# Kernel optimization log

Measured on AMD Instinct MI355X. Metric: run time of the kernel, lower is better.

The kernel has to match this reference:

```python
import jax, jax.numpy as jnp
import numpy as np

B, Q, A, D = 32, 48, 48, 300   # batch, question len, answer len, word embed dim
C, K = 512, 5                  # conv out channels, kernel height
H, P, NCLS = 512, 512, 2       # hidden_size, projection_size, n_classes
EPS_COS = 1e-6
EPS_BN = 1e-5


def _simple_cnn(x, conv_w, conv_b, fc_w, fc_b):
    # x: (N, L, D) -> Conv2d(1->C, kernel=(K, D), padding=(K-1, 0)) -> relu -> maxpool over length -> fc
    y = jax.lax.conv_general_dilated(
        x[:, None, :, :], conv_w, window_strides=(1, 1),
        padding=((K - 1, K - 1), (0, 0)),
        dimension_numbers=('NCHW', 'OIHW', 'NCHW'))  # (N, C, L+K-1, 1)
    y = jax.nn.relu(y + conv_b[None, :, None, None])[..., 0]  # (N, C, L')
    y = jnp.max(y, axis=2)                                    # (N, C)  max_pool1d over full length
    return y @ fc_w.T + fc_b                                  # (N, H)


def setup_inputs() -> dict:
    key = jax.random.key(0)
    ks = jax.random.split(key, 12)
    s = lambda n: 1.0 / np.sqrt(n)
    return {
        'a_features': jax.random.normal(ks[0], (B, Q, D), jnp.float32),
        'b_features': jax.random.normal(ks[1], (B, A, D), jnp.float32),
        'sm_conv_w': jax.random.normal(ks[2], (C, 1, K, D), jnp.float32) * s(K * D),
        'sm_conv_b': jnp.zeros((C,), jnp.float32),
        'sm_fc_w': jax.random.normal(ks[3], (H, C), jnp.float32) * s(C),
        'sm_fc_b': jnp.zeros((H,), jnp.float32),
        'ctx_conv_w': jax.random.normal(ks[4], (C, 1, K, D), jnp.float32) * s(K * D),
        'ctx_conv_b': jnp.zeros((C,), jnp.float32),
        'ctx_fc_w': jax.random.normal(ks[5], (H, C), jnp.float32) * s(C),
        'ctx_fc_b': jnp.zeros((H,), jnp.float32),
        'proj_w': jax.random.normal(ks[6], (P, 3 * H), jnp.float32) * s(3 * H),
        'proj_b': jnp.zeros((P,), jnp.float32),
        'bn_gamma': jnp.ones((P,), jnp.float32),
        'bn_beta': jnp.zeros((P,), jnp.float32),
        'out_w': jax.random.normal(ks[7], (NCLS, P), jnp.float32) * s(P),
        'out_b': jnp.zeros((NCLS,), jnp.float32),
    }


def reference(a_features, b_features, sm_conv_w, sm_conv_b, sm_fc_w, sm_fc_b,
              ctx_conv_w, ctx_conv_b, ctx_fc_w, ctx_fc_b,
              proj_w, proj_b, bn_gamma, bn_beta, out_w, out_b):
    q, a = a_features, b_features
    a_cnn = _simple_cnn(q, sm_conv_w, sm_conv_b, sm_fc_w, sm_fc_b)  # (B, H)
    b_cnn = _simple_cnn(a, sm_conv_w, sm_conv_b, sm_fc_w, sm_fc_b)  # (B, H)

    # attn_context_ave: cosine sim between every (question pos, answer pos) pair
    qn = jnp.linalg.norm(q, axis=-1)                # (B, Q)
    an = jnp.linalg.norm(a, axis=-1)                # (B, A)
    dots = jnp.einsum('bqd,bad->bqa', q, a)
    cos = dots / jnp.maximum(qn[:, :, None] * an[:, None, :], EPS_COS)  # (B, Q, A)
    attn_answer = (a[:, None, :, :] * cos[..., None]).reshape(B * Q, A, D)
    feat = _simple_cnn(attn_answer, ctx_conv_w, ctx_conv_b, ctx_fc_w, ctx_fc_b)
    attn_feat = jnp.mean(feat.reshape(B, Q, H), axis=1)  # sum/Q == mean, (B, H)

    comb = jnp.concatenate([a_cnn, b_cnn, attn_feat], axis=1)  # (B, 3H)
    comb = comb @ proj_w.T + proj_b                            # (B, P)
    # BatchNorm1d in training mode (batch statistics, biased variance)
    mu = jnp.mean(comb, axis=0)
    var = jnp.mean((comb - mu) ** 2, axis=0)
    comb = (comb - mu) / jnp.sqrt(var + EPS_BN) * bn_gamma + bn_beta
    logits = jnp.tanh(comb) @ out_w.T + out_b                  # (B, NCLS)
    return logits
```

## Files before the change

kernel.cpp:

```cpp
#include <hip/hip_runtime.h>
#include <math.h>
#include <stdint.h>

namespace {
constexpr int B = 32, Q = 48, A = 48, D = 300;
constexpr int C = 512, K = 5, H = 512, P = 512, NCLS = 2;
constexpr int CK = C * K;
constexpr int M = B * Q;
constexpr int KP = 320;
constexpr float EPS_COS = 1e-6f, EPS_BN = 1e-5f;
constexpr int NPAN = 96 + 96 + 160 + 160;
constexpr int NCOS = M / 4;
constexpr int NTP  = 768 + 512;
constexpr int NJ = 8;
constexpr int PSZ = 40 * 16 * 8;
}
using short8 = __attribute__((ext_vector_type(8))) short;
using f32x4  = __attribute__((ext_vector_type(4))) float;

__device__ inline short f2bf(float v) {
  uint32_t u = __builtin_bit_cast(uint32_t, v);
  return (short)((u + 0x7fffu + ((u >> 16) & 1u)) >> 16);
}

__global__ void prep_k(const float* __restrict__ q, const float* __restrict__ a,
                       const float* __restrict__ smw, const float* __restrict__ ctxw,
                       const float* __restrict__ projw, const float* __restrict__ smfcw,
                       const float* __restrict__ ctxfcw,
                       short* __restrict__ qb, short* __restrict__ ab,
                       short* __restrict__ smb, short* __restrict__ ctxb,
                       float* __restrict__ projT, float* __restrict__ smfcwT,
                       float* __restrict__ ctxfcwT, float* __restrict__ cosm) {
  __shared__ float sa[16 * 300];
  __shared__ float4 qrow4[300];
  __shared__ float tile[32][33];
  const int vb = blockIdx.x, tid = threadIdx.x;
  if (vb < NPAN) {
    const float* src; short* dst; int pl;
    if (vb < 96)       { src = q;    dst = qb;   pl = vb; }
    else if (vb < 192) { src = a;    dst = ab;   pl = vb - 96; }
    else if (vb < 352) { src = smw;  dst = smb;  pl = vb - 192; }
    else               { src = ctxw; dst = ctxb; pl = vb - 352; }
    const int row0 = pl * 16;
    for (int i = tid; i < 1200; i += 256) {
      const int r = i / 75, c4 = i - r * 75;
      const float4 v = *(const float4*)&src[(size_t)(row0 + r) * D + c4 * 4];
      *(float4*)&sa[r * 300 + c4 * 4] = v;
    }
    __syncthreads();
    for (int it = tid; it < 640; it += 256) {
      const int k8 = it >> 4, r = it & 15;
      short tmp[8];
#pragma unroll
      for (int e = 0; e < 8; ++e) {
        const int k = k8 * 8 + e;
        tmp[e] = (k < D) ? f2bf(sa[r * 300 + k]) : (short)0;
      }
      *(int4*)&dst[(size_t)pl * PSZ + (size_t)k8 * 128 + r * 8] = *(const int4*)tmp;
    }
  } else if (vb < NPAN + NCOS) {
    const int b5 = vb - NPAN;
    const int qq = b5 * 4;
    const int b = qq / Q;
    const float4* qp4 = (const float4*)(q + (size_t)qq * D);
    for (int i = tid; i < 300; i += 256) qrow4[i] = qp4[i];
    __syncthreads();
    const int sub = tid >> 6, lane = tid & 63;
    float qsq = 0.f;
    for (int i = lane; i < 75; i += 64) {
      float4 v = qrow4[sub * 75 + i];
      qsq += v.x * v.x + v.y * v.y + v.z * v.z + v.w * v.w;
    }
#pragma unroll
    for (int off2 = 32; off2; off2 >>= 1) qsq += __shfl_xor(qsq, off2);
    const float qn = sqrtf(qsq);
    if (lane < A) {
      const float4* ap4 = (const float4*)(a + ((size_t)b * A + lane) * D);
      float dot = 0.f, asq = 0.f;
      for (int i = 0; i < 75; ++i) {
        float4 av = ap4[i], qv = qrow4[sub * 75 + i];
        dot += qv.x * av.x + qv.y * av.y + qv.z * av.z + qv.w * av.w;
        asq += av.x * av.x + av.y * av.y + av.z * av.z + av.w * av.w;
      }
      cosm[(size_t)(qq + sub) * A + lane] = dot / fmaxf(qn * sqrtf(asq), EPS_COS);
    }
  } else {
    const int vb2 = vb - NPAN - NCOS;
    const int tx = tid & 31, ty = tid >> 5;
    if (vb2 < 768) {
      const int j0 = (vb2 % 48) * 32, p0 = (vb2 / 48) * 32;
      for (int i = ty; i < 32; i += 8)
        tile[i][tx] = projw[(size_t)(p0 + i) * (3 * H) + j0 + tx];
      __syncthreads();
      for (int i = ty; i < 32; i += 8)
        projT[(size_t)(j0 + i) * P + p0 + tx] = tile[tx][i];
    } else {
      const int b3 = vb2 - 768;
      const bool isC = b3 >= 256;
      const int b4 = isC ? b3 - 256 : b3;
      const float* W = isC ? ctxfcw : smfcw;
      float* WT = isC ? ctxfcwT : smfcwT;
      const int c0 = (b4 % 16) * 32, h0 = (b4 / 16) * 32;
      for (int i = ty; i < 32; i += 8)
        tile[i][tx] = W[(size_t)(h0 + i) * C + c0 + tx];
      __syncthreads();
      for (int i = ty; i < 32; i += 8)
        WT[(size_t)(c0 + i) * H + h0 + tx] = tile[tx][i];
    }
  }
}

__global__ void __launch_bounds__(256)
fused_k(const short* __restrict__ qb, const short* __restrict__ ab,
        const short* __restrict__ smb, const short* __restrict__ ctxb,
        const float* __restrict__ cosm, const float* __restrict__ smbias,
        const float* __restrict__ ctxbias,
        float* __restrict__ pooled, float* __restrict__ pbar) {
  __shared__ __align__(16) char Lraw[80000];
  const int vb = blockIdx.x, tid = threadIdx.x;

  float (*Sl)[56][81] = (float (*)[56][81])Lraw;
  short (*coslb)[56]  = (short (*)[56])(Lraw + 72576);
  float* redf         = (float*)(Lraw + 77952);
  const bool isCtx = vb < 256;
  const int lane = tid & 63, wv = tid >> 6;
  const int r16 = lane & 15, kq = lane >> 4;
  const int v2 = isCtx ? vb : vb - 256;
  const int nb = v2 >> 3, cgi = v2 & 7;

  const short* Xp = isCtx ? ab : ((nb < B) ? qb : ab);
  const int xp0 = (isCtx ? nb : ((nb < B) ? nb : nb - B)) * 3;
  const short* Wp = isCtx ? ctxb : smb;
  const int wp0 = cgi * 20 + wv * 5;
  const short* Xw = Xp + (size_t)xp0 * PSZ + kq * 128 + r16 * 8;
  const short* Ww = Wp + (size_t)wp0 * PSZ + kq * 128 + r16 * 8;

  for (int i = lane; i < 640; i += 64) {
    const int rr = i / 80, cc2 = i % 80;
    Sl[wv][rr < 4 ? rr : rr + 48][cc2] = 0.f;
  }
  if (isCtx) {
    for (int i = tid; i < 48 * 56; i += 256) {
      const int qi = i / 56, p4 = i % 56;
      const float cv = (p4 >= 4 && p4 < 52)
                     ? cosm[((size_t)nb * Q + qi) * A + p4 - 4] : 0.f;
      coslb[qi][p4] = f2bf(cv);
    }
  }

  f32x4 acc[3][5];
#pragma unroll
  for (int mi = 0; mi < 3; ++mi)
#pragma unroll
    for (int ni = 0; ni < 5; ++ni) acc[mi][ni] = f32x4{0.f, 0.f, 0.f, 0.f};

  int4 cA0[3], cB0[5], cA1[3], cB1[5], cA2[3], cB2[5];
  auto issue = [&](int ks, int4* pA, int4* pB) {
#pragma unroll
    for (int i = 0; i < 3; ++i) pA[i] = *(const int4*)(Xw + (size_t)i * PSZ + ks * 512);
#pragma unroll
    for (int i = 0; i < 5; ++i) pB[i] = *(const int4*)(Ww + (size_t)i * PSZ + ks * 512);
  };
  auto domfma = [&](const int4* pA, const int4* pB) {
#pragma unroll
    for (int mi = 0; mi < 3; ++mi)
#pragma unroll
      for (int ni = 0; ni < 5; ++ni)
        acc[mi][ni] = __builtin_amdgcn_mfma_f32_16x16x32_bf16(
            __builtin_bit_cast(short8, pA[mi]),
            __builtin_bit_cast(short8, pB[ni]), acc[mi][ni], 0, 0, 0);
  };

  issue(0, cA0, cB0);
  issue(1, cA1, cB1);
  issue(2, cA2, cB2);
  domfma(cA0, cB0); issue(3, cA0, cB0);
  domfma(cA1, cB1); issue(4, cA1, cB1);
  domfma(cA2, cB2); issue(5, cA2, cB2);
  domfma(cA0, cB0); issue(6, cA0, cB0);
  domfma(cA1, cB1); issue(7, cA1, cB1);
  domfma(cA2, cB2); issue(8, cA2, cB2);
  domfma(cA0, cB0); issue(9, cA0, cB0);
  domfma(cA1, cB1);
  domfma(cA2, cB2);
  domfma(cA0, cB0);

#pragma unroll
  for (int mi = 0; mi < 3; ++mi)
#pragma unroll
    for (int ni = 0; ni < 5; ++ni)
#pragma unroll
      for (int r = 0; r < 4; ++r)
        Sl[wv][mi * 16 + kq * 4 + r + 4][ni * 16 + r16] = acc[mi][ni][r];
  __syncthreads();

  if (!isCtx) {
    const int ch = tid & 63, part = tid >> 6;
    const int w2 = ch >> 4, cl = (ch & 15) * 5;
    float best = -1e30f;
#pragma unroll
    for (int j = 0; j < 13; ++j) {
      const int l = part * 13 + j;
      const float z = Sl[w2][l + 0][cl + 0] + Sl[w2][l + 1][cl + 1]
                    + Sl[w2][l + 2][cl + 2] + Sl[w2][l + 3][cl + 3]
                    + Sl[w2][l + 4][cl + 4];
      best = fmaxf(best, z);
    }
    redf[part * 64 + ch] = best;
    __syncthreads();
    if (tid < 64) {
      const float m = fmaxf(fmaxf(redf[tid], redf[64 + tid]),
                            fmaxf(redf[128 + tid], redf[192 + tid]));
      pooled[(size_t)nb * C + cgi * 64 + tid] =
          fmaxf(m + smbias[cgi * 64 + tid], 0.f);
    }
  } else {
    const int clane = tid & 31, grp = tid >> 5;
    float best[2][6];
#pragma unroll
    for (int cc = 0; cc < 2; ++cc)
#pragma unroll
      for (int j = 0; j < 6; ++j) best[cc][j] = -1e30f;
    for (int ch13 = 0; ch13 < 13; ++ch13) {
      float cw[6][8];
#pragma unroll
      for (int j = 0; j < 6; ++j) {
        const short* crow = &coslb[grp * 6 + j][4 * ch13];
        const int2 w0 = *(const int2*)crow;
        const int2 w1 = *(const int2*)(crow + 4);
        cw[j][0] = __builtin_bit_cast(float, w0.x << 16);
        cw[j][1] = __builtin_bit_cast(float, (int)(w0.x & 0xffff0000));
        cw[j][2] = __builtin_bit_cast(float, w0.y << 16);
        cw[j][3] = __builtin_bit_cast(float, (int)(w0.y & 0xffff0000));
        cw[j][4] = __builtin_bit_cast(float, w1.x << 16);
        cw[j][5] = __builtin_bit_cast(float, (int)(w1.x & 0xffff0000));
        cw[j][6] = __builtin_bit_cast(float, w1.y << 16);
        cw[j][7] = __builtin_bit_cast(float, (int)(w1.y & 0xffff0000));
      }
#pragma unroll
      for (int cc = 0; cc < 2; ++cc) {
        const int ch = cc * 32 + clane;
        const int w2 = ch >> 4, cl = (ch & 15) * 5;
        float sk[4][5];
#pragma unroll
        for (int p = 0; p < 4; ++p)
#pragma unroll
          for (int k = 0; k < K; ++k)
            sk[p][k] = Sl[w2][4 * ch13 + p + k][cl + k];
#pragma unroll
        for (int p = 0; p < 4; ++p)
#pragma unroll
          for (int j = 0; j < 6; ++j) {
            float zv = 0.f;
#pragma unroll
            for (int k = 0; k < K; ++k) zv += cw[j][p + k] * sk[p][k];
            best[cc][j] = fmaxf(best[cc][j], zv);
          }
      }
    }
#pragma unroll
    for (int cc = 0; cc < 2; ++cc) {
      const float bc = ctxbias[cgi * 64 + cc * 32 + clane];
      float s = 0.f;
#pragma unroll
      for (int j = 0; j < 6; ++j) s += fmaxf(best[cc][j] + bc, 0.f);
      redf[cc * 256 + grp * 32 + clane] = s;
    }
    __syncthreads();
    if (tid < 64) {
      const int cc = tid >> 5, cl2 = tid & 31;
      float tot = 0.f;
#pragma unroll
      for (int g = 0; g < 8; ++g) tot += redf[cc * 256 + g * 32 + cl2];
      pbar[(size_t)nb * C + cgi * 64 + cc * 32 + cl2] = tot * (1.0f / Q);
    }
  }
}

__global__ void projfc_k(const float* __restrict__ pooled, const float* __restrict__ pbar,
                         const float* __restrict__ smfcwT, const float* __restrict__ smfcb,
                         const float* __restrict__ ctxfcwT, const float* __restrict__ ctxfcb,
                         const float* __restrict__ projT, float* __restrict__ partial) {
  __shared__ float rows[3 * C];
  __shared__ float cs[192];
  const int b = blockIdx.x, g = blockIdx.y, tid = threadIdx.x;
  for (int i = tid; i < C; i += 256) {
    rows[i] = pooled[(size_t)b * C + i];
    rows[C + i] = pooled[(size_t)(B + b) * C + i];
    rows[2 * C + i] = pbar[(size_t)b * C + i];
  }
  __syncthreads();
  if (tid < 192) {
    const int j = g * 192 + tid;
    const int seg = j >> 9, h = j & 511;
    const float* WT = (seg == 2) ? ctxfcwT : smfcwT;
    const float* in = rows + seg * C;
    float acc = (seg == 2) ? ctxfcb[h] : smfcb[h];
    for (int c = 0; c < C; ++c) acc += in[c] * WT[(size_t)c * H + h];
    cs[tid] = acc;
  }
  __syncthreads();
  const int js = g * 192;
  float a0 = 0.f, a1 = 0.f;
  for (int j = 0; j < 192; ++j) {
    const float c = cs[j];
    a0 += c * projT[(size_t)(js + j) * P + tid];
    a1 += c * projT[(size_t)(js + j) * P + tid + 256];
  }
  partial[((size_t)g * B + b) * P + tid] = a0;
  partial[((size_t)g * B + b) * P + tid + 256] = a1;
}

__global__ void bnmid_k(const float* __restrict__ partial, const float* __restrict__ proj_b,
                        const float* __restrict__ gamma, const float* __restrict__ beta,
                        float* __restrict__ t) {
  __shared__ float s1[256], s2[256];
  const int pl = threadIdx.x & 63, rg = threadIdx.x >> 6;
  const int p = blockIdx.x * 64 + pl;
  const float pb = proj_b[p];
  float v[8];
#pragma unroll
  for (int i = 0; i < 8; ++i) {
    const int r = rg * 8 + i;
    float s = pb;
#pragma unroll
    for (int g = 0; g < NJ; ++g) s += partial[((size_t)g * B + r) * P + p];
    v[i] = s;
  }
  float a = 0.f;
#pragma unroll
  for (int i = 0; i < 8; ++i) a += v[i];
  s1[rg * 64 + pl] = a;
  __syncthreads();
  const float mu = (s1[pl] + s1[64 + pl] + s1[128 + pl] + s1[192 + pl]) * (1.0f / B);
  float b2 = 0.f;
#pragma unroll
  for (int i = 0; i < 8; ++i) { const float d = v[i] - mu; b2 += d * d; }
  s2[rg * 64 + pl] = b2;
  __syncthreads();
  const float var = (s2[pl] + s2[64 + pl] + s2[128 + pl] + s2[192 + pl]) * (1.0f / B);
  const float inv = rsqrtf(var + EPS_BN);
  const float g = gamma[p], be = beta[p];
#pragma unroll
  for (int i = 0; i < 8; ++i)
    t[(size_t)(rg * 8 + i) * P + p] = tanhf((v[i] - mu) * inv * g + be);
}

__global__ void out_k(const float* __restrict__ t, const float* __restrict__ W,
                      const float* __restrict__ bias, float* __restrict__ out) {
  const int tid = threadIdx.x;
  const int o = tid >> 3, lane8 = tid & 7;
  const int bb = o >> 1, cl = o & 1;
  float acc = 0.f;
  for (int j = lane8; j < P; j += 8) acc += t[(size_t)bb * P + j] * W[cl * P + j];
#pragma unroll
  for (int off = 4; off; off >>= 1) acc += __shfl_down(acc, off);
  if (lane8 == 0) out[bb * NCLS + cl] = acc + bias[cl];
}

extern "C" void kernel_launch(void* const* d_in, const int* in_sizes, int n_in,
                              void* d_out, int out_size, void* d_ws, size_t ws_size,
                              hipStream_t stream) {
  const float* q       = (const float*)d_in[0];
  const float* a       = (const float*)d_in[1];
  const float* sm_w    = (const float*)d_in[2];
  const float* sm_b    = (const float*)d_in[3];
  const float* sm_fcw  = (const float*)d_in[4];
  const float* sm_fcb  = (const float*)d_in[5];
  const float* ctx_w   = (const float*)d_in[6];
  const float* ctx_b   = (const float*)d_in[7];
  const float* ctx_fcw = (const float*)d_in[8];
  const float* ctx_fcb = (const float*)d_in[9];
  const float* proj_w  = (const float*)d_in[10];
  const float* proj_b  = (const float*)d_in[11];
  const float* gamma   = (const float*)d_in[12];
  const float* beta    = (const float*)d_in[13];
  const float* out_w   = (const float*)d_in[14];
  const float* out_b   = (const float*)d_in[15];

  float* ws = (float*)d_ws;
  size_t off = 0;
  auto alloc = [&](size_t n) { float* p = ws + off; off += n; return p; };
  float* projT   = alloc((size_t)3 * H * P);
  float* smfcwT  = alloc((size_t)C * H);
  float* ctxfcwT = alloc((size_t)C * H);
  float* cosm    = alloc((size_t)B * Q * A);
  float* pooled  = alloc((size_t)2 * B * C);
  float* pbar    = alloc((size_t)B * C);
  float* partial = alloc((size_t)NJ * B * P);
  float* tbuf    = alloc((size_t)B * P);
  short* qb      = (short*)alloc((size_t)M * KP / 2);
  short* ab      = (short*)alloc((size_t)M * KP / 2);
  short* smb2    = (short*)alloc((size_t)CK * KP / 2);
  short* ctxb2   = (short*)alloc((size_t)CK * KP / 2);

  prep_k<<<NPAN + NCOS + NTP, 256, 0, stream>>>(q, a, sm_w, ctx_w, proj_w, sm_fcw,
                                                ctx_fcw, qb, ab, smb2, ctxb2,
                                                projT, smfcwT, ctxfcwT, cosm);
  fused_k<<<768, 256, 0, stream>>>(qb, ab, smb2, ctxb2, cosm, sm_b, ctx_b,
                                   pooled, pbar);
  projfc_k<<<dim3(B, NJ), 256, 0, stream>>>(pooled, pbar, smfcwT, sm_fcb,
                                            ctxfcwT, ctx_fcb, projT, partial);
  bnmid_k<<<P / 64, 256, 0, stream>>>(partial, proj_b, gamma, beta, tbuf);
  out_k<<<1, 512, 0, stream>>>(tbuf, out_w, out_b, (float*)d_out);
}
```

Baseline: 83.39 us.

## Fuse projection, batchnorm and output kernels into one cooperative kernel

Replaces the three tail kernels (fc+projection partials, batchnorm+tanh, output linear) with a single cooperative launch of 256 blocks that separates the stages with grid.sync(). This removes two kernel launch boundaries and their dispatch gaps. In exchange it adds grid-wide barrier cost and cooperative-launch overhead, and leaves most blocks idle during the later stages.

```diff
diff --git a/kernel.cpp b/kernel.cpp
--- a/kernel.cpp
+++ b/kernel.cpp
@@ -1,6 +1,9 @@
 #include <hip/hip_runtime.h>
+#include <hip/hip_cooperative_groups.h>
 #include <math.h>
 #include <stdint.h>
+
+namespace cg = cooperative_groups;
 
 namespace {
 constexpr int B = 32, Q = 48, A = 48, D = 300;
@@ -277,85 +280,92 @@
   }
 }
 
-__global__ void projfc_k(const float* __restrict__ pooled, const float* __restrict__ pbar,
-                         const float* __restrict__ smfcwT, const float* __restrict__ smfcb,
-                         const float* __restrict__ ctxfcwT, const float* __restrict__ ctxfcb,
-                         const float* __restrict__ projT, float* __restrict__ partial) {
+struct TailArgs {
+  const float *pooled, *pbar, *smfcwT, *smfcb, *ctxfcwT, *ctxfcb, *projT;
+  const float *projb, *gamma, *beta, *outw, *outb;
+  float *partial, *tbuf, *out;
+};
+
+__global__ void __launch_bounds__(256) tail_k(TailArgs Ar) {
   __shared__ float rows[3 * C];
-  __shared__ float cs[192];
-  const int b = blockIdx.x, g = blockIdx.y, tid = threadIdx.x;
-  for (int i = tid; i < C; i += 256) {
-    rows[i] = pooled[(size_t)b * C + i];
-    rows[C + i] = pooled[(size_t)(B + b) * C + i];
-    rows[2 * C + i] = pbar[(size_t)b * C + i];
-  }
-  __syncthreads();
-  if (tid < 192) {
-    const int j = g * 192 + tid;
-    const int seg = j >> 9, h = j & 511;
-    const float* WT = (seg == 2) ? ctxfcwT : smfcwT;
-    const float* in = rows + seg * C;
-    float acc = (seg == 2) ? ctxfcb[h] : smfcb[h];
-    for (int c = 0; c < C; ++c) acc += in[c] * WT[(size_t)c * H + h];
-    cs[tid] = acc;
-  }
-  __syncthreads();
-  const int js = g * 192;
-  float a0 = 0.f, a1 = 0.f;
-  for (int j = 0; j < 192; ++j) {
-    const float c = cs[j];
-    a0 += c * projT[(size_t)(js + j) * P + tid];
-    a1 += c * projT[(size_t)(js + j) * P + tid + 256];
-  }
-  partial[((size_t)g * B + b) * P + tid] = a0;
-  partial[((size_t)g * B + b) * P + tid + 256] = a1;
-}
-
-__global__ void bnmid_k(const float* __restrict__ partial, const float* __restrict__ proj_b,
-                        const float* __restrict__ gamma, const float* __restrict__ beta,
-                        float* __restrict__ t) {
-  __shared__ float s1[256], s2[256];
-  const int pl = threadIdx.x & 63, rg = threadIdx.x >> 6;
-  const int p = blockIdx.x * 64 + pl;
-  const float pb = proj_b[p];
-  float v[8];
-#pragma unroll
-  for (int i = 0; i < 8; ++i) {
-    const int r = rg * 8 + i;
-    float s = pb;
-#pragma unroll
-    for (int g = 0; g < NJ; ++g) s += partial[((size_t)g * B + r) * P + p];
-    v[i] = s;
-  }
-  float a = 0.f;
-#pragma unroll
-  for (int i = 0; i < 8; ++i) a += v[i];
-  s1[rg * 64 + pl] = a;
-  __syncthreads();
-  const float mu = (s1[pl] + s1[64 + pl] + s1[128 + pl] + s1[192 + pl]) * (1.0f / B);
-  float b2 = 0.f;
-#pragma unroll
-  for (int i = 0; i < 8; ++i) { const float d = v[i] - mu; b2 += d * d; }
-  s2[rg * 64 + pl] = b2;
-  __syncthreads();
-  const float var = (s2[pl] + s2[64 + pl] + s2[128 + pl] + s2[192 + pl]) * (1.0f / B);
-  const float inv = rsqrtf(var + EPS_BN);
-  const float g = gamma[p], be = beta[p];
-#pragma unroll
-  for (int i = 0; i < 8; ++i)
-    t[(size_t)(rg * 8 + i) * P + p] = tanhf((v[i] - mu) * inv * g + be);
-}
-
-__global__ void out_k(const float* __restrict__ t, const float* __restrict__ W,
-                      const float* __restrict__ bias, float* __restrict__ out) {
+  __shared__ float cs[256];
+  __shared__ float s2[256];
+  cg::grid_group grid = cg::this_grid();
   const int tid = threadIdx.x;
-  const int o = tid >> 3, lane8 = tid & 7;
-  const int bb = o >> 1, cl = o & 1;
-  float acc = 0.f;
-  for (int j = lane8; j < P; j += 8) acc += t[(size_t)bb * P + j] * W[cl * P + j];
-#pragma unroll
-  for (int off = 4; off; off >>= 1) acc += __shfl_down(acc, off);
-  if (lane8 == 0) out[bb * NCLS + cl] = acc + bias[cl];
+
+  {
+    const int b = blockIdx.x >> 3, g = blockIdx.x & 7;
+    for (int i = tid; i < C; i += 256) {
+      rows[i] = Ar.pooled[(size_t)b * C + i];
+      rows[C + i] = Ar.pooled[(size_t)(B + b) * C + i];
+      rows[2 * C + i] = Ar.pbar[(size_t)b * C + i];
+    }
+    __syncthreads();
+    if (tid < 192) {
+      const int j = g * 192 + tid;
+      const int seg = j >> 9, h = j & 511;
+      const float* WT = (seg == 2) ? Ar.ctxfcwT : Ar.smfcwT;
+      const float* in = rows + seg * C;
+      float acc = (seg == 2) ? Ar.ctxfcb[h] : Ar.smfcb[h];
+      for (int c = 0; c < C; ++c) acc += in[c] * WT[(size_t)c * H + h];
+      cs[tid] = acc;
+    }
+    __syncthreads();
+    const int js = g * 192;
+    float a0 = 0.f, a1 = 0.f;
+    for (int j = 0; j < 192; ++j) {
+      const float c = cs[j];
+      a0 += c * Ar.projT[(size_t)(js + j) * P + tid];
+      a1 += c * Ar.projT[(size_t)(js + j) * P + tid + 256];
+    }
+    Ar.partial[((size_t)g * B + b) * P + tid] = a0;
+    Ar.partial[((size_t)g * B + b) * P + tid + 256] = a1;
+  }
+  grid.sync();
+
+  if (blockIdx.x < 8) {
+    const int pl = tid & 63, rg = tid >> 6;
+    const int p = blockIdx.x * 64 + pl;
+    const float pb = Ar.projb[p];
+    float v[8];
+#pragma unroll
+    for (int i = 0; i < 8; ++i) {
+      const int r = rg * 8 + i;
+      float s = pb;
+#pragma unroll
+      for (int g = 0; g < NJ; ++g) s += Ar.partial[((size_t)g * B + r) * P + p];
+      v[i] = s;
+    }
+    float a = 0.f;
+#pragma unroll
+    for (int i = 0; i < 8; ++i) a += v[i];
+    cs[rg * 64 + pl] = a;
+    __syncthreads();
+    const float mu = (cs[pl] + cs[64 + pl] + cs[128 + pl] + cs[192 + pl]) * (1.0f / B);
+    float b2 = 0.f;
+#pragma unroll
+    for (int i = 0; i < 8; ++i) { const float d = v[i] - mu; b2 += d * d; }
+    s2[rg * 64 + pl] = b2;
+    __syncthreads();
+    const float var = (s2[pl] + s2[64 + pl] + s2[128 + pl] + s2[192 + pl]) * (1.0f / B);
+    const float inv = rsqrtf(var + EPS_BN);
+    const float g = Ar.gamma[p], be = Ar.beta[p];
+#pragma unroll
+    for (int i = 0; i < 8; ++i)
+      Ar.tbuf[(size_t)(rg * 8 + i) * P + p] = tanhf((v[i] - mu) * inv * g + be);
+  }
+  grid.sync();
+
+  if (blockIdx.x == 0) {
+    const int o = tid >> 2, lane4 = tid & 3;
+    const int bb = o >> 1, cl = o & 1;
+    float acc = 0.f;
+    for (int j = lane4; j < P; j += 4)
+      acc += Ar.tbuf[(size_t)bb * P + j] * Ar.outw[cl * P + j];
+    acc += __shfl_down(acc, 2, 4);
+    acc += __shfl_down(acc, 1, 4);
+    if (lane4 == 0) Ar.out[bb * NCLS + cl] = acc + Ar.outb[cl];
+  }
 }
 
 extern "C" void kernel_launch(void* const* d_in, const int* in_sizes, int n_in,
@@ -399,8 +409,15 @@
                                                 projT, smfcwT, ctxfcwT, cosm);
   fused_k<<<768, 256, 0, stream>>>(qb, ab, smb2, ctxb2, cosm, sm_b, ctx_b,
                                    pooled, pbar);
-  projfc_k<<<dim3(B, NJ), 256, 0, stream>>>(pooled, pbar, smfcwT, sm_fcb,
-                                            ctxfcwT, ctx_fcb, projT, partial);
-  bnmid_k<<<P / 64, 256, 0, stream>>>(partial, proj_b, gamma, beta, tbuf);
-  out_k<<<1, 512, 0, stream>>>(tbuf, out_w, out_b, (float*)d_out);
-}
+  TailArgs Ta;
+  Ta.pooled = pooled; Ta.pbar = pbar;
+  Ta.smfcwT = smfcwT; Ta.smfcb = sm_fcb;
+  Ta.ctxfcwT = ctxfcwT; Ta.ctxfcb = ctx_fcb;
+  Ta.projT = projT; Ta.projb = proj_b;
+  Ta.gamma = gamma; Ta.beta = beta;
+  Ta.outw = out_w; Ta.outb = out_b;
+  Ta.partial = partial; Ta.tbuf = tbuf; Ta.out = (float*)d_out;
+  void* kargs[] = {(void*)&Ta};
+  hipLaunchCooperativeKernel((const void*)tail_k, dim3(256), dim3(256),
+                             kargs, 0, stream);
+}
```

Result: slower. 145.9 us (+74.9%).
